# Kernel tuning notes

Measured on AMD Instinct MI355X. Metric: run time of the kernel, lower is better.

## Reference

```python
import jax, jax.numpy as jnp
import numpy as np

B, N, E, F_IN, F_OUT, F_EDGE = 8, 1024, 1536, 64, 64, 32


def _build_graph(seed=0):
    rng = np.random.default_rng(seed)
    src = rng.integers(0, N, size=E)
    off = rng.integers(1, N, size=E)
    dst = (src + off) % N  # guaranteed distinct from src
    inc = np.zeros((N, E), dtype=np.float32)
    inc[src, np.arange(E)] = 1.0
    inc[dst, np.arange(E)] = 1.0
    adj = np.zeros((N, N), dtype=np.float32)
    adj[src, dst] = 1.0
    adj[dst, src] = 1.0
    adj_sl = adj + np.eye(N, dtype=np.float32)
    deg = adj_sl.sum(axis=1)
    dinv = (1.0 / np.sqrt(deg)).astype(np.float32)  # D^{-1/2}, diag
    lap = (dinv[:, None] * adj_sl * dinv[None, :]).astype(np.float32)
    return inc, lap


def setup_inputs() -> dict:
    key = jax.random.key(0)
    k1, k2, k3, k4 = jax.random.split(key, 4)
    inc, lap = _build_graph()
    return {
        "nodes": jax.random.normal(k1, (B, N, F_IN), dtype=jnp.float32),
        "edges": jax.random.normal(k2, (B, E, F_EDGE), dtype=jnp.float32),
        "weight_matrix": jax.random.normal(k3, (F_IN, F_OUT), dtype=jnp.float32),
        "edge_weight_vec": jax.random.normal(k4, (F_EDGE,), dtype=jnp.float32),
        "inc_matrix": jnp.asarray(inc),
        "norm_symm_laplacian": jnp.asarray(lap),
    }


def reference(nodes, edges, weight_matrix, edge_weight_vec, inc_matrix, norm_symm_laplacian):
    # edge feature reduction: [B,E,F_e] @ [F_e] -> [B,E]
    ew = jnp.einsum("bef,f->be", edges, edge_weight_vec)
    # TDT[b,i,j] = sum_e over edges incident to BOTH i and j of ew[b,e].
    # This replaces the original per-(i,j) Python-dict gather loop with one
    # fused contraction over the binary incidence mask.
    incb = (inc_matrix != 0).astype(ew.dtype)           # [N,E]
    tmp = incb[None, :, :] * ew[:, None, :]             # [B,N,E]
    tdt = jnp.einsum("bie,je->bij", tmp, incb)          # [B,N,N]
    a_mat = tdt * norm_symm_laplacian                   # elementwise with D^-1/2(A+I)D^-1/2
    h = nodes @ weight_matrix                           # [B,N,F_out]
    return jnp.einsum("bij,bjf->bif", a_mat, h)         # [B,N,F_out]
```

## Files before the change

kernel.cpp:

```cpp
#include <hip/hip_runtime.h>

#define B_ 8
#define N_ 1024
#define E_ 1536
#define FIN_ 64
#define FOUT_ 64
#define FEDGE_ 32
#define CAP_ 32

#define WS_DEG   0
#define WS_ADJ   4096
#define WS_LAPUV 266240
#define WS_EW    272384
#define WS_H     321536

#define NT_BLOCKS 2048
#define EX_BLOCKS 96
#define EW_BLOCKS 48
#define K1_BLOCKS (NT_BLOCKS + EX_BLOCKS + EW_BLOCKS)

__global__ __launch_bounds__(256) void fused_prep(
    const float* __restrict__ nodes,
    const float* __restrict__ W,
    const float* __restrict__ inc,
    const float* __restrict__ edges,
    const float* __restrict__ evec,
    const float* __restrict__ lap,
    int*   __restrict__ deg,
    int2*  __restrict__ adj,
    float* __restrict__ lapuv,
    float* __restrict__ ew,
    float* __restrict__ h)
{
    __shared__ float Wt[FOUT_ * 68];
    __shared__ float rows[4 * FIN_];
    __shared__ int smin[16], smax[16];
    const int blk = blockIdx.x;
    const int tid = threadIdx.x;

    if (blk < NT_BLOCKS) {
#pragma unroll
        for (int idx = tid; idx < FIN_ * FOUT_; idx += 256) {
            Wt[(idx & 63) * 68 + (idx >> 6)] = W[idx];
        }
        rows[tid] = nodes[(size_t)blk * 256 + tid];
        __syncthreads();
        const int r = tid >> 6;
        const int f = tid & 63;
        const float4* wp = (const float4*)&Wt[f * 68];
        const float4* xp = (const float4*)&rows[r * FIN_];
        float acc = 0.0f;
#pragma unroll
        for (int q = 0; q < FIN_ / 4; ++q) {
            const float4 w = wp[q];
            const float4 x = xp[q];
            acc += w.x * x.x + w.y * x.y + w.z * x.z + w.w * x.w;
        }
        h[(size_t)blk * 256 + tid] = acc;
    } else if (blk < NT_BLOCKS + EX_BLOCKS) {
        const int c0 = (blk - NT_BLOCKS) * 16;
        if (tid < 16) { smin[tid] = 0x7fffffff; smax[tid] = -1; }
        __syncthreads();
        const int col = tid & 15;
        const int rb  = tid >> 4;
        int lmin = 0x7fffffff, lmax = -1;
        const float* p = inc + (size_t)rb * E_ + c0 + col;
#pragma unroll 4
        for (int i = 0; i < N_ / 16; ++i) {
            if (p[(size_t)i * 16 * E_] != 0.0f) {
                const int r = rb + 16 * i;
                lmin = min(lmin, r);
                lmax = max(lmax, r);
            }
        }
        if (lmax >= 0) {
            atomicMin(&smin[col], lmin);
            atomicMax(&smax[col], lmax);
        }
        __syncthreads();
        if (tid < 16) {
            const int e = c0 + tid;
            const int u = smin[tid];
            const int v = smax[tid];
            const int pu = atomicAdd(&deg[u], 1);
            if (pu < CAP_) adj[u * CAP_ + pu] = make_int2(v, e);
            const int pv = atomicAdd(&deg[v], 1);
            if (pv < CAP_) adj[v * CAP_ + pv] = make_int2(u, e);
            lapuv[e] = lap[(size_t)u * N_ + v];
        }
    } else {
        const int t = (blk - NT_BLOCKS - EX_BLOCKS) * 256 + tid;
        const float4* ep = (const float4*)(edges + (size_t)t * FEDGE_);
        float s = 0.0f;
#pragma unroll
        for (int j = 0; j < FEDGE_ / 4; ++j) {
            const float4 a = ep[j];
            s += a.x * evec[4 * j + 0] + a.y * evec[4 * j + 1]
               + a.z * evec[4 * j + 2] + a.w * evec[4 * j + 3];
        }
        ew[t] = s;
    }
}

__global__ __launch_bounds__(256) void gather_nodes(
    const int*   __restrict__ deg,
    const int2*  __restrict__ adj,
    const float* __restrict__ lapuv,
    const float* __restrict__ ew,
    const float* __restrict__ lap,
    const float* __restrict__ h,
    float*       __restrict__ out)
{
    const int wid  = (blockIdx.x * 256 + threadIdx.x) >> 6;
    const int lane = threadIdx.x & 63;
    const int b = wid >> 10;
    const int u = wid & (N_ - 1);
    int d = deg[u];
    if (d > CAP_) d = CAP_;
    const float* hb  = h + (size_t)b * N_ * FOUT_;
    const float* ewb = ew + (size_t)b * E_;
    float acc = 0.0f, esum = 0.0f;
    for (int j = 0; j < d; ++j) {
        const int2 a = adj[u * CAP_ + j];
        const float s = ewb[a.y];
        acc  += s * lapuv[a.y] * hb[(size_t)a.x * FOUT_ + lane];
        esum += s;
    }
    const float ldiag = lap[(size_t)u * (N_ + 1)];
    out[(size_t)wid * FOUT_ + lane] =
        acc + esum * ldiag * hb[(size_t)u * FOUT_ + lane];
}

extern "C" void kernel_launch(void* const* d_in, const int* in_sizes, int n_in,
                              void* d_out, int out_size, void* d_ws, size_t ws_size,
                              hipStream_t stream) {
    const float* nodes = (const float*)d_in[0];
    const float* edges = (const float*)d_in[1];
    const float* W     = (const float*)d_in[2];
    const float* evec  = (const float*)d_in[3];
    const float* inc   = (const float*)d_in[4];
    const float* lap   = (const float*)d_in[5];
    float* out = (float*)d_out;

    char* ws = (char*)d_ws;
    int*   deg   = (int*)(ws + WS_DEG);
    int2*  adj   = (int2*)(ws + WS_ADJ);
    float* lapuv = (float*)(ws + WS_LAPUV);
    float* ewb   = (float*)(ws + WS_EW);
    float* h     = (float*)(ws + WS_H);

    hipMemsetAsync(deg, 0, N_ * sizeof(int), stream);

    fused_prep<<<K1_BLOCKS, 256, 0, stream>>>(nodes, W, inc, edges, evec, lap,
                                              deg, adj, lapuv, ewb, h);
    gather_nodes<<<(B_ * N_ * FOUT_) / 256, 256, 0, stream>>>(deg, adj, lapuv, ewb,
                                                              lap, h, out);
}
```

Baseline: 91.97 us.

## Aggregate raw node features before weight projection and compute edge weights inline

The prep kernel is reduced to building the adjacency lists from the incidence matrix, now with 512 threads per block. The gather kernel aggregates raw input features first and applies W afterwards, using associativity. Edge weights are computed on the fly with a wave shuffle reduction, and Laplacian entries are read directly. This drops the h, ew and lapuv intermediate buffers and their global round trips, but it recomputes the edge dot products once per batch and node endpoint, and it adds a per-block load of W into shared memory.

Measured after the change: 89.69 us. 1.03x faster.

```diff
diff --git a/kernel.cpp b/kernel.cpp
--- a/kernel.cpp
+++ b/kernel.cpp
@@ -8,127 +8,101 @@
 #define FEDGE_ 32
 #define CAP_ 32
 
-#define WS_DEG   0
-#define WS_ADJ   4096
-#define WS_LAPUV 266240
-#define WS_EW    272384
-#define WS_H     321536
+#define WS_DEG 0
+#define WS_ADJ 4096
 
-#define NT_BLOCKS 2048
-#define EX_BLOCKS 96
-#define EW_BLOCKS 48
-#define K1_BLOCKS (NT_BLOCKS + EX_BLOCKS + EW_BLOCKS)
-
-__global__ __launch_bounds__(256) void fused_prep(
-    const float* __restrict__ nodes,
-    const float* __restrict__ W,
+__global__ __launch_bounds__(512) void build_csr(
     const float* __restrict__ inc,
-    const float* __restrict__ edges,
-    const float* __restrict__ evec,
-    const float* __restrict__ lap,
-    int*   __restrict__ deg,
-    int2*  __restrict__ adj,
-    float* __restrict__ lapuv,
-    float* __restrict__ ew,
-    float* __restrict__ h)
+    int*  __restrict__ deg,
+    int2* __restrict__ adj)
 {
-    __shared__ float Wt[FOUT_ * 68];
-    __shared__ float rows[4 * FIN_];
     __shared__ int smin[16], smax[16];
-    const int blk = blockIdx.x;
     const int tid = threadIdx.x;
-
-    if (blk < NT_BLOCKS) {
-#pragma unroll
-        for (int idx = tid; idx < FIN_ * FOUT_; idx += 256) {
-            Wt[(idx & 63) * 68 + (idx >> 6)] = W[idx];
+    const int c0 = blockIdx.x * 16;
+    if (tid < 16) { smin[tid] = 0x7fffffff; smax[tid] = -1; }
+    __syncthreads();
+    const int col = tid & 15;
+    const int rb  = tid >> 4;
+    int lmin = 0x7fffffff, lmax = -1;
+    const float* p = inc + (size_t)rb * E_ + c0 + col;
+#pragma unroll 8
+    for (int i = 0; i < N_ / 32; ++i) {
+        if (p[(size_t)i * 32 * E_] != 0.0f) {
+            const int r = rb + 32 * i;
+            lmin = min(lmin, r);
+            lmax = max(lmax, r);
         }
-        rows[tid] = nodes[(size_t)blk * 256 + tid];
-        __syncthreads();
-        const int r = tid >> 6;
-        const int f = tid & 63;
-        const float4* wp = (const float4*)&Wt[f * 68];
-        const float4* xp = (const float4*)&rows[r * FIN_];
-        float acc = 0.0f;
-#pragma unroll
-        for (int q = 0; q < FIN_ / 4; ++q) {
-            const float4 w = wp[q];
-            const float4 x = xp[q];
-            acc += w.x * x.x + w.y * x.y + w.z * x.z + w.w * x.w;
-        }
-        h[(size_t)blk * 256 + tid] = acc;
-    } else if (blk < NT_BLOCKS + EX_BLOCKS) {
-        const int c0 = (blk - NT_BLOCKS) * 16;
-        if (tid < 16) { smin[tid] = 0x7fffffff; smax[tid] = -1; }
-        __syncthreads();
-        const int col = tid & 15;
-        const int rb  = tid >> 4;
-        int lmin = 0x7fffffff, lmax = -1;
-        const float* p = inc + (size_t)rb * E_ + c0 + col;
-#pragma unroll 4
-        for (int i = 0; i < N_ / 16; ++i) {
-            if (p[(size_t)i * 16 * E_] != 0.0f) {
-                const int r = rb + 16 * i;
-                lmin = min(lmin, r);
-                lmax = max(lmax, r);
-            }
-        }
-        if (lmax >= 0) {
-            atomicMin(&smin[col], lmin);
-            atomicMax(&smax[col], lmax);
-        }
-        __syncthreads();
-        if (tid < 16) {
-            const int e = c0 + tid;
-            const int u = smin[tid];
-            const int v = smax[tid];
-            const int pu = atomicAdd(&deg[u], 1);
-            if (pu < CAP_) adj[u * CAP_ + pu] = make_int2(v, e);
-            const int pv = atomicAdd(&deg[v], 1);
-            if (pv < CAP_) adj[v * CAP_ + pv] = make_int2(u, e);
-            lapuv[e] = lap[(size_t)u * N_ + v];
-        }
-    } else {
-        const int t = (blk - NT_BLOCKS - EX_BLOCKS) * 256 + tid;
-        const float4* ep = (const float4*)(edges + (size_t)t * FEDGE_);
-        float s = 0.0f;
-#pragma unroll
-        for (int j = 0; j < FEDGE_ / 4; ++j) {
-            const float4 a = ep[j];
-            s += a.x * evec[4 * j + 0] + a.y * evec[4 * j + 1]
-               + a.z * evec[4 * j + 2] + a.w * evec[4 * j + 3];
-        }
-        ew[t] = s;
+    }
+    if (lmax >= 0) {
+        atomicMin(&smin[col], lmin);
+        atomicMax(&smax[col], lmax);
+    }
+    __syncthreads();
+    if (tid < 16) {
+        const int e = c0 + tid;
+        const int u = smin[tid];
+        const int v = smax[tid];
+        const int pu = atomicAdd(&deg[u], 1);
+        if (pu < CAP_) adj[u * CAP_ + pu] = make_int2(v, e);
+        const int pv = atomicAdd(&deg[v], 1);
+        if (pv < CAP_) adj[v * CAP_ + pv] = make_int2(u, e);
     }
 }
 
-__global__ __launch_bounds__(256) void gather_nodes(
+__global__ __launch_bounds__(256) void gather_all(
+    const float* __restrict__ nodes,
+    const float* __restrict__ edges,
+    const float* __restrict__ W,
+    const float* __restrict__ evec,
+    const float* __restrict__ lap,
     const int*   __restrict__ deg,
     const int2*  __restrict__ adj,
-    const float* __restrict__ lapuv,
-    const float* __restrict__ ew,
-    const float* __restrict__ lap,
-    const float* __restrict__ h,
     float*       __restrict__ out)
 {
-    const int wid  = (blockIdx.x * 256 + threadIdx.x) >> 6;
-    const int lane = threadIdx.x & 63;
+    __shared__ float Wt[FOUT_ * 68];
+    __shared__ float xs[4][FIN_];
+    const int tid = threadIdx.x;
+#pragma unroll
+    for (int idx = tid; idx < FIN_ * FOUT_; idx += 256)
+        Wt[(idx & 63) * 68 + (idx >> 6)] = W[idx];
+
+    const int w    = tid >> 6;
+    const int lane = tid & 63;
+    const int wid  = blockIdx.x * 4 + w;
     const int b = wid >> 10;
     const int u = wid & (N_ - 1);
     int d = deg[u];
     if (d > CAP_) d = CAP_;
-    const float* hb  = h + (size_t)b * N_ * FOUT_;
-    const float* ewb = ew + (size_t)b * E_;
-    float acc = 0.0f, esum = 0.0f;
+    const float* nb = nodes + (size_t)b * N_ * FIN_;
+    const float  ev = evec[lane & 31];
+    float xagg = 0.0f, esum = 0.0f;
     for (int j = 0; j < d; ++j) {
         const int2 a = adj[u * CAP_ + j];
-        const float s = ewb[a.y];
-        acc  += s * lapuv[a.y] * hb[(size_t)a.x * FOUT_ + lane];
-        esum += s;
+        float pe = edges[((size_t)b * E_ + a.y) * FEDGE_ + (lane & 31)] * ev;
+        pe += __shfl_xor(pe, 16);
+        pe += __shfl_xor(pe, 8);
+        pe += __shfl_xor(pe, 4);
+        pe += __shfl_xor(pe, 2);
+        pe += __shfl_xor(pe, 1);
+        const float luv = lap[(size_t)u * N_ + a.x];
+        xagg += pe * luv * nb[(size_t)a.x * FIN_ + lane];
+        esum += pe;
     }
     const float ldiag = lap[(size_t)u * (N_ + 1)];
-    out[(size_t)wid * FOUT_ + lane] =
-        acc + esum * ldiag * hb[(size_t)u * FOUT_ + lane];
+    xagg += esum * ldiag * nb[(size_t)u * FIN_ + lane];
+
+    xs[w][lane] = xagg;
+    __syncthreads();
+    const float4* xp = (const float4*)&xs[w][0];
+    const float4* wp = (const float4*)&Wt[lane * 68];
+    float acc = 0.0f;
+#pragma unroll
+    for (int q = 0; q < FIN_ / 4; ++q) {
+        const float4 x  = xp[q];
+        const float4 wv = wp[q];
+        acc += x.x * wv.x + x.y * wv.y + x.z * wv.z + x.w * wv.w;
+    }
+    out[(size_t)wid * FOUT_ + lane] = acc;
 }
 
 extern "C" void kernel_launch(void* const* d_in, const int* in_sizes, int n_in,
@@ -143,16 +117,11 @@
     float* out = (float*)d_out;
 
     char* ws = (char*)d_ws;
-    int*   deg   = (int*)(ws + WS_DEG);
-    int2*  adj   = (int2*)(ws + WS_ADJ);
-    float* lapuv = (float*)(ws + WS_LAPUV);
-    float* ewb   = (float*)(ws + WS_EW);
-    float* h     = (float*)(ws + WS_H);
+    int*  deg = (int*)(ws + WS_DEG);
+    int2* adj = (int2*)(ws + WS_ADJ);
 
     hipMemsetAsync(deg, 0, N_ * sizeof(int), stream);
-
-    fused_prep<<<K1_BLOCKS, 256, 0, stream>>>(nodes, W, inc, edges, evec, lap,
-                                              deg, adj, lapuv, ewb, h);
-    gather_nodes<<<(B_ * N_ * FOUT_) / 256, 256, 0, stream>>>(deg, adj, lapuv, ewb,
-                                                              lap, h, out);
+    build_csr<<<E_ / 16, 512, 0, stream>>>(inc, deg, adj);
+    gather_all<<<(B_ * N_) / 4, 256, 0, stream>>>(nodes, edges, W, evec, lap,
+                                                  deg, adj, out);
 }
```
